# Kernel optimization log

Hardware: AMD Instinct MI355X
Metric: run time of the kernel (lower is better)

Reference implementation:

```python
import jax, jax.numpy as jnp
import numpy as np

D_MODEL = 1024
HEAD_SIZE = 64

def setup_inputs() -> dict:
    key = jax.random.key(0)
    ks = jax.random.split(key, 7)
    s = 1.0 / np.sqrt(D_MODEL)
    return {
        "x": jax.random.normal(ks[0], (4, 2048, D_MODEL), dtype=jnp.float32),
        "wq": jax.random.uniform(ks[1], (D_MODEL, HEAD_SIZE), jnp.float32, -s, s),
        "bq": jax.random.uniform(ks[2], (HEAD_SIZE,), jnp.float32, -s, s),
        "wk": jax.random.uniform(ks[3], (D_MODEL, HEAD_SIZE), jnp.float32, -s, s),
        "bk": jax.random.uniform(ks[4], (HEAD_SIZE,), jnp.float32, -s, s),
        "wv": jax.random.uniform(ks[5], (D_MODEL, HEAD_SIZE), jnp.float32, -s, s),
        "bv": jax.random.uniform(ks[6], (HEAD_SIZE,), jnp.float32, -s, s),
    }

def reference(x, wq, bq, wk, bk, wv, bv):
    # x: [b, n, d_model]; projections -> [b, n, head_size]
    q = x @ wq + bq
    k = x @ wk + bk
    v = x @ wv + bv
    scores = jnp.einsum("bnd,bmd->bnm", q, k) / jnp.sqrt(jnp.float32(HEAD_SIZE))
    attn = jax.nn.softmax(scores, axis=-1)  # [b, n, n]
    return jnp.einsum("bnm,bmd->bnd", attn, v)
```

## Files before the change

### kernel.cpp

```cpp
#include <hip/hip_runtime.h>
#include <math.h>

#define D_MODEL 1024
#define HEAD 64
#define SEQ 2048
#define BATCH 4

typedef _Float16 f16x4 __attribute__((ext_vector_type(4)));
typedef _Float16 f16x8 __attribute__((ext_vector_type(8)));
typedef float f32x4 __attribute__((ext_vector_type(4)));

__global__ __launch_bounds__(256) void prep_w(
    const float* __restrict__ wq, const float* __restrict__ wk,
    const float* __restrict__ wv, _Float16* __restrict__ wT)
{
    const float* w = (blockIdx.y == 0) ? wq : (blockIdx.y == 1) ? wk : wv;
    const int kbase = blockIdx.x * 64;
    __shared__ float t[64][65];
    const int tid = threadIdx.x;
    #pragma unroll
    for (int i = 0; i < 16; i++) {
        int idx = tid + i * 256;
        int kk = idx >> 6, c = idx & 63;
        t[kk][c] = w[(size_t)(kbase + kk) * 64 + c];
    }
    __syncthreads();
    #pragma unroll
    for (int i = 0; i < 16; i++) {
        int idx = tid + i * 256;
        int c = idx >> 6, kk = idx & 63;
        wT[(size_t)(blockIdx.y * 64 + c) * 1024 + kbase + kk] = (_Float16)t[kk][c];
    }
}

__global__ __launch_bounds__(768, 6) void proj_kernel(
    const float* __restrict__ x, const _Float16* __restrict__ wT,
    const float* __restrict__ bq, const float* __restrict__ bk2,
    const float* __restrict__ bv,
    _Float16* __restrict__ q, _Float16* __restrict__ k, _Float16* __restrict__ vT)
{
    const int tid = threadIdx.x;
    const int wave = tid >> 6;
    const int lane = tid & 63;
    const int l16 = lane & 15;
    const int quad = lane >> 4;
    const int row0 = blockIdx.x * 16;

    __shared__ __align__(16) _Float16 Xs[2][16][136];

    const int srow = tid >> 5;
    const int sc4 = tid & 31;
    const float4* xg = reinterpret_cast<const float4*>(x)
                     + (size_t)(row0 + srow) * (D_MODEL / 4) + sc4;

    float4 xr;
    if (tid < 512) xr = xg[0];

    const _Float16* wp = wT + (size_t)(wave * 16 + l16) * D_MODEL + quad * 8;

    f32x4 acc = (f32x4){0.f, 0.f, 0.f, 0.f};

    #pragma unroll
    for (int c = 0; c < 8; c++) {
        if (tid < 512) {
            f16x4 h;
            h[0] = (_Float16)xr.x; h[1] = (_Float16)xr.y;
            h[2] = (_Float16)xr.z; h[3] = (_Float16)xr.w;
            *(f16x4*)&Xs[c & 1][srow][sc4 * 4] = h;
            if (c < 7) xr = xg[(c + 1) * 32];
        }
        __syncthreads();
        #pragma unroll
        for (int kw = 0; kw < 4; kw++) {
            f16x8 aX = *(const f16x8*)&Xs[c & 1][l16][kw * 32 + quad * 8];
            f16x8 bW = *(const f16x8*)(wp + c * 128 + kw * 32);
            acc = __builtin_amdgcn_mfma_f32_16x16x32_f16(aX, bW, acc, 0, 0, 0);
        }
    }

    const int g = wave * 16 + l16;
    const int batch = row0 / SEQ;
    const int rbase = row0 + quad * 4;
    if (g < 64) {
        float bias = bq[g];
        #pragma unroll
        for (int r = 0; r < 4; r++)
            q[(size_t)(rbase + r) * HEAD + g] = (_Float16)((acc[r] + bias) * 0.125f);
    } else if (g < 128) {
        float bias = bk2[g - 64];
        #pragma unroll
        for (int r = 0; r < 4; r++)
            k[(size_t)(rbase + r) * HEAD + (g - 64)] = (_Float16)(acc[r] + bias);
    } else {
        float bias = bv[g - 128];
        f16x4 pk;
        #pragma unroll
        for (int r = 0; r < 4; r++) pk[r] = (_Float16)(acc[r] + bias);
        const int seq0 = row0 - batch * SEQ + quad * 4;
        *(f16x4*)(vT + (size_t)(batch * HEAD + (g - 128)) * SEQ + seq0) = pk;
    }
}

__global__ __launch_bounds__(512, 2) void attn_kernel(
    const _Float16* __restrict__ q, const _Float16* __restrict__ k,
    const _Float16* __restrict__ vT, float* __restrict__ out)
{
    const int tid = threadIdx.x;
    const int wave = tid >> 6;
    const int lane = tid & 63;
    const int l16 = lane & 15;
    const int quad = lane >> 4;
    const int b = blockIdx.y;
    const int q0 = blockIdx.x * 16;

    __shared__ __align__(16) char SM[128 * 72 * 2 + 64 * 136 * 2];
    _Float16 (*Ks)[72] = (_Float16(*)[72])SM;
    _Float16 (*Vs)[136] = (_Float16(*)[136])(SM + 128 * 72 * 2);
    float (*Oall)[16][68] = (float(*)[16][68])SM;
    __shared__ float Lall[8][16];

    f16x8 bQ[2];
    {
        const _Float16* qp = q + (size_t)(b * SEQ + q0 + l16) * HEAD + quad * 8;
        bQ[0] = *(const f16x8*)qp;
        bQ[1] = *(const f16x8*)(qp + 32);
    }

    f32x4 O[4];
    #pragma unroll
    for (int dt = 0; dt < 4; dt++) O[dt] = (f32x4){0.f, 0.f, 0.f, 0.f};
    float lpart = 0.f;

    const _Float16* kb = k + (size_t)b * SEQ * HEAD;
    const _Float16* vb = vT + (size_t)b * HEAD * SEQ;

    const int krow = tid >> 3, kc8 = (tid & 7) * 8;
    const int vrow = tid >> 4, vc8 = (tid & 15) * 8;
    const _Float16* kg = kb + (size_t)krow * HEAD + kc8;
    const _Float16* vg = vb + (size_t)vrow * SEQ + vc8;

    f16x8 kr0 = *(const f16x8*)kg;
    f16x8 kr1 = *(const f16x8*)(kg + (size_t)64 * HEAD);
    f16x8 vr0 = *(const f16x8*)vg;
    f16x8 vr1 = *(const f16x8*)(vg + (size_t)32 * SEQ);

    for (int kc = 0; kc < SEQ; kc += 128) {
        *(f16x8*)&Ks[krow][kc8] = kr0;
        *(f16x8*)&Ks[krow + 64][kc8] = kr1;
        *(f16x8*)&Vs[vrow][vc8] = vr0;
        *(f16x8*)&Vs[vrow + 32][vc8] = vr1;
        if (kc + 128 < SEQ) {
            kr0 = *(const f16x8*)(kg + (size_t)(kc + 128) * HEAD);
            kr1 = *(const f16x8*)(kg + (size_t)(kc + 192) * HEAD);
            vr0 = *(const f16x8*)(vg + kc + 128);
            vr1 = *(const f16x8*)(vg + (size_t)32 * SEQ + kc + 128);
        }
        __syncthreads();

        f16x8 aK0 = *(const f16x8*)&Ks[wave * 16 + l16][quad * 8];
        f16x8 aK1 = *(const f16x8*)&Ks[wave * 16 + l16][32 + quad * 8];
        f32x4 st = __builtin_amdgcn_mfma_f32_16x16x32_f16(aK0, bQ[0], (f32x4){0.f, 0.f, 0.f, 0.f}, 0, 0, 0);
        st = __builtin_amdgcn_mfma_f32_16x16x32_f16(aK1, bQ[1], st, 0, 0, 0);

        float p0 = __expf(st[0]);
        float p1 = __expf(st[1]);
        float p2 = __expf(st[2]);
        float p3 = __expf(st[3]);
        lpart += (p0 + p1) + (p2 + p3);
        f16x4 bP;
        bP[0] = (_Float16)p0; bP[1] = (_Float16)p1;
        bP[2] = (_Float16)p2; bP[3] = (_Float16)p3;

        #pragma unroll
        for (int dt = 0; dt < 4; dt++) {
            f16x4 aV = *(const f16x4*)&Vs[dt * 16 + l16][wave * 16 + quad * 4];
            O[dt] = __builtin_amdgcn_mfma_f32_16x16x16f16(aV, bP, O[dt], 0, 0, 0);
        }
        __syncthreads();
    }

    lpart += __shfl_xor(lpart, 16);
    lpart += __shfl_xor(lpart, 32);
    if (lane < 16) Lall[wave][l16] = lpart;
    #pragma unroll
    for (int dt = 0; dt < 4; dt++)
        #pragma unroll
        for (int r = 0; r < 4; r++)
            Oall[wave][l16][dt * 16 + quad * 4 + r] = O[dt][r];
    __syncthreads();

    {
        int qi = tid >> 5;
        int dd = (tid & 31) * 2;
        float L = 0.f, o0 = 0.f, o1 = 0.f;
        #pragma unroll
        for (int w = 0; w < 8; w++) {
            L += Lall[w][qi];
            o0 += Oall[w][qi][dd];
            o1 += Oall[w][qi][dd + 1];
        }
        float inv = 1.f / L;
        float2 res = make_float2(o0 * inv, o1 * inv);
        *(float2*)(out + (size_t)(b * SEQ + q0 + qi) * HEAD + dd) = res;
    }
}

extern "C" void kernel_launch(void* const* d_in, const int* in_sizes, int n_in,
                              void* d_out, int out_size, void* d_ws, size_t ws_size,
                              hipStream_t stream) {
    const float* x  = (const float*)d_in[0];
    const float* wq = (const float*)d_in[1];
    const float* bq = (const float*)d_in[2];
    const float* wk = (const float*)d_in[3];
    const float* bk = (const float*)d_in[4];
    const float* wv = (const float*)d_in[5];
    const float* bv = (const float*)d_in[6];
    float* out = (float*)d_out;

    const size_t proj_elems = (size_t)BATCH * SEQ * HEAD;
    _Float16* qh = (_Float16*)d_ws;
    _Float16* kh = qh + proj_elems;
    _Float16* vT = kh + proj_elems;
    _Float16* wT = vT + proj_elems;

    prep_w<<<dim3(16, 3), 256, 0, stream>>>(wq, wk, wv, wT);
    proj_kernel<<<dim3(BATCH * SEQ / 16), 768, 0, stream>>>(x, wT, bq, bk, bv, qh, kh, vT);
    attn_kernel<<<dim3(SEQ / 16, BATCH), 512, 0, stream>>>(qh, kh, vT, out);
}
```

Measured before the change: 125.5 us.

## Double-buffer K/V tiles in attention and restructure projection prefetch loop

The attention kernel now keeps two LDS buffers for K and V tiles. This cuts each iteration to a single barrier, and the next tile's global loads are issued before the current tile's MFMAs and stored into the other buffer afterward. The projection kernel's loop is reorganized the same way: it loads weights and the next X chunk up front, writes converted X into the alternate buffer after the MFMAs, and disables unrolling. Launch bounds for attention rise to 4 blocks per SM, while doubled LDS (about 70KB per block) may limit the occupancy actually reached.

Result: no change. 124.0 us (-1.2%).

```diff
diff --git a/kernel.cpp b/kernel.cpp
--- a/kernel.cpp
+++ b/kernel.cpp
@@ -53,28 +53,41 @@
     const float4* xg = reinterpret_cast<const float4*>(x)
                      + (size_t)(row0 + srow) * (D_MODEL / 4) + sc4;
 
+    const _Float16* wp = wT + (size_t)(wave * 16 + l16) * D_MODEL + quad * 8;
+
     float4 xr;
-    if (tid < 512) xr = xg[0];
-
-    const _Float16* wp = wT + (size_t)(wave * 16 + l16) * D_MODEL + quad * 8;
+    if (tid < 512) {
+        xr = xg[0];
+        f16x4 h;
+        h[0] = (_Float16)xr.x; h[1] = (_Float16)xr.y;
+        h[2] = (_Float16)xr.z; h[3] = (_Float16)xr.w;
+        *(f16x4*)&Xs[0][srow][sc4 * 4] = h;
+    }
 
     f32x4 acc = (f32x4){0.f, 0.f, 0.f, 0.f};
 
-    #pragma unroll
+    #pragma unroll 1
     for (int c = 0; c < 8; c++) {
-        if (tid < 512) {
+        __syncthreads();
+        f16x8 bw0 = *(const f16x8*)(wp + c * 128);
+        f16x8 bw1 = *(const f16x8*)(wp + c * 128 + 32);
+        f16x8 bw2 = *(const f16x8*)(wp + c * 128 + 64);
+        f16x8 bw3 = *(const f16x8*)(wp + c * 128 + 96);
+        if (c < 7 && tid < 512) xr = xg[(c + 1) * 32];
+        const int bsel = c & 1;
+        f16x8 aX0 = *(const f16x8*)&Xs[bsel][l16][0 * 32 + quad * 8];
+        f16x8 aX1 = *(const f16x8*)&Xs[bsel][l16][1 * 32 + quad * 8];
+        f16x8 aX2 = *(const f16x8*)&Xs[bsel][l16][2 * 32 + quad * 8];
+        f16x8 aX3 = *(const f16x8*)&Xs[bsel][l16][3 * 32 + quad * 8];
+        acc = __builtin_amdgcn_mfma_f32_16x16x32_f16(aX0, bw0, acc, 0, 0, 0);
+        acc = __builtin_amdgcn_mfma_f32_16x16x32_f16(aX1, bw1, acc, 0, 0, 0);
+        acc = __builtin_amdgcn_mfma_f32_16x16x32_f16(aX2, bw2, acc, 0, 0, 0);
+        acc = __builtin_amdgcn_mfma_f32_16x16x32_f16(aX3, bw3, acc, 0, 0, 0);
+        if (c < 7 && tid < 512) {
             f16x4 h;
             h[0] = (_Float16)xr.x; h[1] = (_Float16)xr.y;
             h[2] = (_Float16)xr.z; h[3] = (_Float16)xr.w;
-            *(f16x4*)&Xs[c & 1][srow][sc4 * 4] = h;
-            if (c < 7) xr = xg[(c + 1) * 32];
-        }
-        __syncthreads();
-        #pragma unroll
-        for (int kw = 0; kw < 4; kw++) {
-            f16x8 aX = *(const f16x8*)&Xs[c & 1][l16][kw * 32 + quad * 8];
-            f16x8 bW = *(const f16x8*)(wp + c * 128 + kw * 32);
-            acc = __builtin_amdgcn_mfma_f32_16x16x32_f16(aX, bW, acc, 0, 0, 0);
+            *(f16x4*)&Xs[bsel ^ 1][srow][sc4 * 4] = h;
         }
     }
 
@@ -101,7 +114,7 @@
     }
 }
 
-__global__ __launch_bounds__(512, 2) void attn_kernel(
+__global__ __launch_bounds__(512, 4) void attn_kernel(
     const _Float16* __restrict__ q, const _Float16* __restrict__ k,
     const _Float16* __restrict__ vT, float* __restrict__ out)
 {
@@ -113,9 +126,9 @@
     const int b = blockIdx.y;
     const int q0 = blockIdx.x * 16;
 
-    __shared__ __align__(16) char SM[128 * 72 * 2 + 64 * 136 * 2];
-    _Float16 (*Ks)[72] = (_Float16(*)[72])SM;
-    _Float16 (*Vs)[136] = (_Float16(*)[136])(SM + 128 * 72 * 2);
+    __shared__ __align__(16) char SM[2 * 18432 + 2 * 17408];
+    _Float16 (*Ks)[128][72] = (_Float16(*)[128][72])SM;
+    _Float16 (*Vs)[64][136] = (_Float16(*)[64][136])(SM + 2 * 18432);
     float (*Oall)[16][68] = (float(*)[16][68])SM;
     __shared__ float Lall[8][16];
 
@@ -143,22 +156,24 @@
     f16x8 kr1 = *(const f16x8*)(kg + (size_t)64 * HEAD);
     f16x8 vr0 = *(const f16x8*)vg;
     f16x8 vr1 = *(const f16x8*)(vg + (size_t)32 * SEQ);
-
-    for (int kc = 0; kc < SEQ; kc += 128) {
-        *(f16x8*)&Ks[krow][kc8] = kr0;
-        *(f16x8*)&Ks[krow + 64][kc8] = kr1;
-        *(f16x8*)&Vs[vrow][vc8] = vr0;
-        *(f16x8*)&Vs[vrow + 32][vc8] = vr1;
-        if (kc + 128 < SEQ) {
-            kr0 = *(const f16x8*)(kg + (size_t)(kc + 128) * HEAD);
-            kr1 = *(const f16x8*)(kg + (size_t)(kc + 192) * HEAD);
-            vr0 = *(const f16x8*)(vg + kc + 128);
-            vr1 = *(const f16x8*)(vg + (size_t)32 * SEQ + kc + 128);
-        }
+    *(f16x8*)&Ks[0][krow][kc8] = kr0;
+    *(f16x8*)&Ks[0][krow + 64][kc8] = kr1;
+    *(f16x8*)&Vs[0][vrow][vc8] = vr0;
+    *(f16x8*)&Vs[0][vrow + 32][vc8] = vr1;
+
+    #pragma unroll 1
+    for (int c = 0; c < 16; c++) {
         __syncthreads();
-
-        f16x8 aK0 = *(const f16x8*)&Ks[wave * 16 + l16][quad * 8];
-        f16x8 aK1 = *(const f16x8*)&Ks[wave * 16 + l16][32 + quad * 8];
+        if (c < 15) {
+            const int kc2 = (c + 1) * 128;
+            kr0 = *(const f16x8*)(kg + (size_t)kc2 * HEAD);
+            kr1 = *(const f16x8*)(kg + (size_t)(kc2 + 64) * HEAD);
+            vr0 = *(const f16x8*)(vg + kc2);
+            vr1 = *(const f16x8*)(vg + (size_t)32 * SEQ + kc2);
+        }
+        const int bsel = c & 1;
+        f16x8 aK0 = *(const f16x8*)&Ks[bsel][wave * 16 + l16][quad * 8];
+        f16x8 aK1 = *(const f16x8*)&Ks[bsel][wave * 16 + l16][32 + quad * 8];
         f32x4 st = __builtin_amdgcn_mfma_f32_16x16x32_f16(aK0, bQ[0], (f32x4){0.f, 0.f, 0.f, 0.f}, 0, 0, 0);
         st = __builtin_amdgcn_mfma_f32_16x16x32_f16(aK1, bQ[1], st, 0, 0, 0);
 
@@ -173,11 +188,17 @@
 
         #pragma unroll
         for (int dt = 0; dt < 4; dt++) {
-            f16x4 aV = *(const f16x4*)&Vs[dt * 16 + l16][wave * 16 + quad * 4];
+            f16x4 aV = *(const f16x4*)&Vs[bsel][dt * 16 + l16][wave * 16 + quad * 4];
             O[dt] = __builtin_amdgcn_mfma_f32_16x16x16f16(aV, bP, O[dt], 0, 0, 0);
         }
-        __syncthreads();
-    }
+        if (c < 15) {
+            *(f16x8*)&Ks[bsel ^ 1][krow][kc8] = kr0;
+            *(f16x8*)&Ks[bsel ^ 1][krow + 64][kc8] = kr1;
+            *(f16x8*)&Vs[bsel ^ 1][vrow][vc8] = vr0;
+            *(f16x8*)&Vs[bsel ^ 1][vrow + 32][vc8] = vr1;
+        }
+    }
+    __syncthreads();
 
     lpart += __shfl_xor(lpart, 16);
     lpart += __shfl_xor(lpart, 32);
```
